# Performance work log

Measured on AMD Instinct MI355X. Metric: run time of the kernel, lower is better.

## Reference

```python
import jax, jax.numpy as jnp
import numpy as np

EPS = 1e-5
STEPS = 4
MULTIPLIER = 4
CROP_SHIFT = 4  # deterministic stand-in for RandomCrop: translate by 4px


def _box_blur(x):
    # 3x3 box blur, reflect padding (kornia RandomBoxBlur default), shape-preserving
    H, W = x.shape[-2], x.shape[-1]
    xp = jnp.pad(x, ((0, 0), (0, 0), (1, 1), (1, 1)), mode='reflect')
    acc = xp[..., 0:H, 0:W]
    for i in range(3):
        for j in range(3):
            if i == 0 and j == 0:
                continue
            acc = acc + xp[..., i:i + H, j:j + W]
    return acc / 9.0


def _mixed_op(h, w):
    # weighted sum over the 7 DA_2D_PRIMITIVES (deterministic versions):
    # none, blur, invert, hflip, vflip, crop(translate), rotate(90 deg)
    return (w[0] * h
            + w[1] * _box_blur(h)
            + w[2] * (1.0 - h)
            + w[3] * jnp.flip(h, axis=-1)
            + w[4] * jnp.flip(h, axis=-2)
            + w[5] * jnp.roll(h, shift=(CROP_SHIFT, CROP_SHIFT), axis=(-2, -1))
            + w[6] * jnp.rot90(h, k=1, axes=(-2, -1)))


def _cell(s0, s1, weights):
    states = [s0, s1]
    offset = 0
    for i in range(STEPS):
        s = states[0] * 0.0
        for j, h in enumerate(states):
            s = s + _mixed_op(h, weights[offset + j])
        offset += len(states)
        states.append(s)
    return jnp.concatenate(states[-MULTIPLIER:], axis=1)


def setup_inputs() -> dict:
    key = jax.random.key(0)
    k1, k2, k3 = jax.random.split(key, 3)
    B, C, H, W = 16, 48, 128, 128
    return {
        'x': jax.random.normal(k1, (B, C, H, W), dtype=jnp.float32),
        'gamma': jnp.ones((C,), dtype=jnp.float32),
        'beta': jnp.zeros((C,), dtype=jnp.float32),
        'alphas_normal': 0.001 * jax.random.normal(k2, (14, 7), dtype=jnp.float32),
        'alphas_reduce': 0.001 * jax.random.normal(k3, (14, 7), dtype=jnp.float32),
    }


def reference(x, gamma, beta, alphas_normal, alphas_reduce):
    # stem: BatchNorm2d in training mode (batch statistics)
    mean = jnp.mean(x, axis=(0, 2, 3), keepdims=True)
    var = jnp.var(x, axis=(0, 2, 3), keepdims=True)
    s = (x - mean) * jax.lax.rsqrt(var + EPS)
    s = s * gamma[None, :, None, None] + beta[None, :, None, None]
    # layers=1: cell 0 is a reduction cell -> uses alphas_reduce
    w = jax.nn.softmax(alphas_reduce, axis=-1)  # [14 edges, 7 ops]
    return _cell(s, s, w)
```

## Files before the change

### kernel.cpp

```cpp
#include <hip/hip_runtime.h>
#include <math.h>

#define NCH 48
#define NB 16
#define PLANE 16384
#define NPLANES 768

#define WS_PSUM  0
#define WS_PSQ   768
#define WS_SCALE 1536
#define WS_SHIFT 1584
#define WS_TAB   1632
#define WS_CONST 1728

typedef _Float16 h2 __attribute__((ext_vector_type(2)));

__global__ __launch_bounds__(256) void stats_kernel(const float* __restrict__ x,
                                                    float* __restrict__ ws) {
  int p = blockIdx.x;
  int t = threadIdx.x;
  const float4* x4 = (const float4*)x + (size_t)p * 4096;
  float s = 0.f, q = 0.f;
  #pragma unroll
  for (int k = 0; k < 16; ++k) {
    float4 v = x4[k * 256 + t];
    s += v.x + v.y + v.z + v.w;
    q += v.x * v.x + v.y * v.y + v.z * v.z + v.w * v.w;
  }
  #pragma unroll
  for (int off = 32; off > 0; off >>= 1) {
    s += __shfl_xor(s, off, 64);
    q += __shfl_xor(q, off, 64);
  }
  __shared__ float red[8];
  int wid = t >> 6, lane = t & 63;
  if (lane == 0) { red[wid] = s; red[4 + wid] = q; }
  __syncthreads();
  if (t == 0) {
    ws[WS_PSUM + p] = red[0] + red[1] + red[2] + red[3];
    ws[WS_PSQ  + p] = red[4] + red[5] + red[6] + red[7];
  }
}

__global__ void prep_kernel(const float* __restrict__ gamma, const float* __restrict__ beta,
                            const float* __restrict__ alphas, float* __restrict__ ws) {
  int t = threadIdx.x;
  if (t < NCH) {
    float s = 0.f, q = 0.f;
    for (int b = 0; b < NB; ++b) {
      s += ws[WS_PSUM + b * NCH + t];
      q += ws[WS_PSQ  + b * NCH + t];
    }
    const float inv = 1.0f / ((float)NB * PLANE);
    float mean = s * inv;
    float var  = q * inv - mean * mean;
    float sc = gamma[t] * rsqrtf(var + 1e-5f);
    ws[WS_SCALE + t] = sc;
    ws[WS_SHIFT + t] = beta[t] - mean * sc;
  }
  if (t == 0) {
    float w[14][7];
    for (int r = 0; r < 14; ++r) {
      float m = -1e30f;
      for (int k = 0; k < 7; ++k) m = fmaxf(m, alphas[r * 7 + k]);
      float sum = 0.f;
      for (int k = 0; k < 7; ++k) { float e = expf(alphas[r * 7 + k] - m); w[r][k] = e; sum += e; }
      float is = 1.0f / sum;
      for (int k = 0; k < 7; ++k) w[r][k] *= is;
    }
    for (int i = 0; i < 96; ++i) ws[WS_TAB + i] = 0.f;
    for (int i = 0; i < 4;  ++i) ws[WS_CONST + i] = 0.f;
    const int map[14][2] = {
      {0,0},{0,0},
      {0,1},{0,1},{1,1},
      {0,2},{0,2},{1,2},{2,2},
      {0,3},{0,3},{1,3},{2,3},{3,3}
    };
    for (int r = 0; r < 14; ++r) {
      int p = map[r][0], tg = map[r][1];
      float* cf = ws + WS_TAB + (p * 4 + tg) * 6;
      cf[0] += w[r][0] - w[r][2];
      cf[1] += w[r][1] * (1.0f / 9.0f);
      cf[2] += w[r][3];
      cf[3] += w[r][4];
      cf[4] += w[r][5];
      cf[5] += w[r][6];
      ws[WS_CONST + tg] += w[r][2];
    }
  }
}


__device__ __forceinline__ float ldshw(const h2* L, int i, int j) {
  int q = (j >> 2) ^ (i & 31);
  h2 p = L[(i << 6) + (q << 1) + ((j & 2) >> 1)];
  return (j & 1) ? (float)p.y : (float)p.x;
}

#define RDQ(L, I, B, M) {                                                      \
  int q_ = (B) ^ ((I) & 31);                                                   \
  h2 p0_ = (L)[((I) << 6) + (q_ << 1)];                                        \
  h2 p1_ = (L)[((I) << 6) + (q_ << 1) + 1];                                    \
  M.x = (float)p0_.x; M.y = (float)p0_.y;                                      \
  M.z = (float)p1_.x; M.w = (float)p1_.y; }

#define WRQ(L, I, B, V) {                                                      \
  int q_ = (B) ^ ((I) & 31);                                                   \
  h2 p0_, p1_;                                                                 \
  p0_.x = (_Float16)V.x; p0_.y = (_Float16)V.y;                                \
  p1_.x = (_Float16)V.z; p1_.y = (_Float16)V.w;                                \
  (L)[((I) << 6) + (q_ << 1)] = p0_;                                           \
  (L)[((I) << 6) + (q_ << 1) + 1] = p1_; }

#define HROW(h, m, lo, hi)                                                     \
  h.x = lo + m.x + m.y; h.y = m.x + m.y + m.z;                                 \
  h.z = m.y + m.z + m.w; h.w = m.z + m.w + hi;

#define FMA4(T, C, M)                                                          \
  T.x += (C) * M.x; T.y += (C) * M.y; T.z += (C) * M.z; T.w += (C) * M.w;

#define BLUR4(T, A, B, Cq)                                                     \
  T.x += c1 * (A.x + B.x + Cq.x); T.y += c1 * (A.y + B.y + Cq.y);              \
  T.z += c1 * (A.z + B.z + Cq.z); T.w += c1 * (A.w + B.w + Cq.w);

#define FLIPL(T, M)                                                            \
  T.x += c2 * M.w; T.y += c2 * M.z; T.z += c2 * M.y; T.w += c2 * M.x;

#define GATHER(L, OI, TYC) {                                                   \
  float4 m, hA, hB, hC; float lo, hi; int ri;                                  \
                                                                      \
  ri = ((OI) == 0) ? 1 : (OI) - 1;                                             \
  RDQ(L, ri, tx, m) lo = ldshw(L, ri, cLo); hi = ldshw(L, ri, cHi);            \
  HROW(hA, m, lo, hi)                                                          \
                                                                      \
  RDQ(L, (OI), tx, m) lo = ldshw(L, (OI), cLo); hi = ldshw(L, (OI), cHi);      \
  FMA4(T0, c0, m)                                                              \
  HROW(hB, m, lo, hi)                                                          \
                                                                      \
  RDQ(L, (OI)+1, tx, m) lo = ldshw(L, (OI)+1, cLo); hi = ldshw(L, (OI)+1, cHi);\
  FMA4(T1, c0, m)                                                              \
  HROW(hC, m, lo, hi)                                                          \
  BLUR4(T0, hA, hB, hC)                                                        \
                                                                      \
  RDQ(L, (OI)+2, tx, m) lo = ldshw(L, (OI)+2, cLo); hi = ldshw(L, (OI)+2, cHi);\
  FMA4(T2, c0, m)                                                              \
  HROW(hA, m, lo, hi)                                                          \
  BLUR4(T1, hB, hC, hA)                                                        \
                                                                      \
  RDQ(L, (OI)+3, tx, m) lo = ldshw(L, (OI)+3, cLo); hi = ldshw(L, (OI)+3, cHi);\
  FMA4(T3, c0, m)                                                              \
  HROW(hB, m, lo, hi)                                                          \
  BLUR4(T2, hC, hA, hB)                                                        \
                                                                      \
  ri = ((OI) == 124) ? 126 : (OI) + 4;                                         \
  RDQ(L, ri, tx, m) lo = ldshw(L, ri, cLo); hi = ldshw(L, ri, cHi);            \
  HROW(hC, m, lo, hi)                                                          \
  BLUR4(T3, hA, hB, hC)                                                        \
                                                                   \
  RDQ(L, (OI),   31 - tx, m) FLIPL(T0, m)                                      \
  RDQ(L, (OI)+1, 31 - tx, m) FLIPL(T1, m)                                      \
  RDQ(L, (OI)+2, 31 - tx, m) FLIPL(T2, m)                                      \
  RDQ(L, (OI)+3, 31 - tx, m) FLIPL(T3, m)                                      \
                                                                   \
  RDQ(L, 127 - (OI), tx, m) FMA4(T0, c3, m)                                    \
  RDQ(L, 126 - (OI), tx, m) FMA4(T1, c3, m)                                    \
  RDQ(L, 125 - (OI), tx, m) FMA4(T2, c3, m)                                    \
  RDQ(L, 124 - (OI), tx, m) FMA4(T3, c3, m)                                    \
                                                              \
  RDQ(L, ((OI) - 4) & 127, rc, m) FMA4(T0, c4, m)                              \
  RDQ(L, ((OI) - 3) & 127, rc, m) FMA4(T1, c4, m)                              \
  RDQ(L, ((OI) - 2) & 127, rc, m) FMA4(T2, c4, m)                              \
  RDQ(L, ((OI) - 1) & 127, rc, m) FMA4(T3, c4, m)                              \
                                     \
  RDQ(L, oj,     31 - (TYC), m)                                                \
  T0.x += c5 * m.w; T1.x += c5 * m.z; T2.x += c5 * m.y; T3.x += c5 * m.x;      \
  RDQ(L, oj + 1, 31 - (TYC), m)                                                \
  T0.y += c5 * m.w; T1.y += c5 * m.z; T2.y += c5 * m.y; T3.y += c5 * m.x;      \
  RDQ(L, oj + 2, 31 - (TYC), m)                                                \
  T0.z += c5 * m.w; T1.z += c5 * m.z; T2.z += c5 * m.y; T3.z += c5 * m.x;      \
  RDQ(L, oj + 3, 31 - (TYC), m)                                                \
  T0.w += c5 * m.w; T1.w += c5 * m.z; T2.w += c5 * m.y; T3.w += c5 * m.x;      \
}

#define LDCF(P, TG) {                                                          \
  const float* cfp = wsf + WS_TAB + ((P) * 4 + (TG)) * 6;                      \
  c0 = cfp[0]; c1 = cfp[1]; c2 = cfp[2]; c3 = cfp[3]; c4 = cfp[4]; c5 = cfp[5]; }

#define SETC(K) {                                                              \
  float cst = wsf[WS_CONST + (K)];                                             \
  T0.x = cst; T0.y = cst; T0.z = cst; T0.w = cst; T1 = T0; T2 = T0; T3 = T0; }

#define STAGE_BN(L, OI) {                                                      \
  float4 v;                                                                    \
  v = x4[((OI)+0)*32 + tx]; v.x = v.x*sc+sh; v.y = v.y*sc+sh; v.z = v.z*sc+sh; \
  v.w = v.w*sc+sh; WRQ(L, (OI)+0, tx, v)                                       \
  v = x4[((OI)+1)*32 + tx]; v.x = v.x*sc+sh; v.y = v.y*sc+sh; v.z = v.z*sc+sh; \
  v.w = v.w*sc+sh; WRQ(L, (OI)+1, tx, v)                                       \
  v = x4[((OI)+2)*32 + tx]; v.x = v.x*sc+sh; v.y = v.y*sc+sh; v.z = v.z*sc+sh; \
  v.w = v.w*sc+sh; WRQ(L, (OI)+2, tx, v)                                       \
  v = x4[((OI)+3)*32 + tx]; v.x = v.x*sc+sh; v.y = v.y*sc+sh; v.z = v.z*sc+sh; \
  v.w = v.w*sc+sh; WRQ(L, (OI)+3, tx, v) }

#define STAGE_OUT(L, TG, OI) {                                                 \
  float4 v;                                                                    \
  v = out4[(pbase + (TG)*NCH)*4096 + ((OI)+0)*32 + tx]; WRQ(L, (OI)+0, tx, v)  \
  v = out4[(pbase + (TG)*NCH)*4096 + ((OI)+1)*32 + tx]; WRQ(L, (OI)+1, tx, v)  \
  v = out4[(pbase + (TG)*NCH)*4096 + ((OI)+2)*32 + tx]; WRQ(L, (OI)+2, tx, v)  \
  v = out4[(pbase + (TG)*NCH)*4096 + ((OI)+3)*32 + tx]; WRQ(L, (OI)+3, tx, v) }

#define WRITEV(TG, OI) {                                                       \
  out4[(pbase + (TG)*NCH)*4096 + ((OI)+0)*32 + tx] = T0;                       \
  out4[(pbase + (TG)*NCH)*4096 + ((OI)+1)*32 + tx] = T1;                       \
  out4[(pbase + (TG)*NCH)*4096 + ((OI)+2)*32 + tx] = T2;                       \
  out4[(pbase + (TG)*NCH)*4096 + ((OI)+3)*32 + tx] = T3; }

#define LOADV(TG, OI) {                                                        \
  T0 = out4[(pbase + (TG)*NCH)*4096 + ((OI)+0)*32 + tx];                       \
  T1 = out4[(pbase + (TG)*NCH)*4096 + ((OI)+1)*32 + tx];                       \
  T2 = out4[(pbase + (TG)*NCH)*4096 + ((OI)+2)*32 + tx];                       \
  T3 = out4[(pbase + (TG)*NCH)*4096 + ((OI)+3)*32 + tx]; }

#define STASHV(L, OI) {                                                        \
  WRQ(L, (OI)+0, tx, T0) WRQ(L, (OI)+1, tx, T1)                                \
  WRQ(L, (OI)+2, tx, T2) WRQ(L, (OI)+3, tx, T3) }

__global__ __launch_bounds__(256, 1)
void main_kernel(const float* __restrict__ x,
                 const float* __restrict__ wsf, float* out)
{
  __shared__ h2 lds[2 * 8192];
  h2* h0 = lds;
  h2* h1 = lds + 8192;
  int bx = blockIdx.x;
  int b = bx / NCH, c = bx % NCH;
  int tid = threadIdx.x;
  int ty = tid >> 5, tx = tid & 31;
  int oj = tx << 2;
  int cLo = (tx == 0)  ? 1   : oj - 1;
  int cHi = (tx == 31) ? 126 : oj + 4;
  int rc  = (tx + 31) & 31;
  float4* out4 = (float4*)out;
  const size_t pbase = (size_t)b * 192 + c;
  const float4* x4 = (const float4*)x + (size_t)bx * 4096;
  float sc = wsf[WS_SCALE + c], sh = wsf[WS_SHIFT + c];

  float4 T0, T1, T2, T3;
  float c0, c1, c2, c3, c4, c5;

  #pragma unroll 1
  for (int k = 0; k < 4; ++k) {
    int oi = (ty + 8 * k) << 2;
    STAGE_BN(h0, oi);
  }
  __syncthreads();

  #pragma unroll 1
  for (int k = 0; k < 4; ++k) {
    int oi = (ty + 8 * k) << 2; int tyc = ty + 8 * k;
    SETC(0); LDCF(0, 0);
    GATHER(h0, oi, tyc);
    WRITEV(0, oi);
    STASHV(h1, oi);
  }
  __syncthreads();

  #pragma unroll 1
  for (int k = 0; k < 4; ++k) {
    int oi = (ty + 8 * k) << 2; int tyc = ty + 8 * k;
    SETC(1); LDCF(0, 1); GATHER(h0, oi, tyc);
             LDCF(1, 1); GATHER(h1, oi, tyc);
    WRITEV(1, oi);
    SETC(2); LDCF(0, 2); GATHER(h0, oi, tyc);
             LDCF(1, 2); GATHER(h1, oi, tyc);
    WRITEV(2, oi);
    SETC(3); LDCF(0, 3); GATHER(h0, oi, tyc);
             LDCF(1, 3); GATHER(h1, oi, tyc);
    WRITEV(3, oi);
  }
  __syncthreads();

  #pragma unroll 1
  for (int k = 0; k < 4; ++k) {
    int oi = (ty + 8 * k) << 2;
    STAGE_OUT(h0, 1, oi);
  }
  __syncthreads();

  #pragma unroll 1
  for (int k = 0; k < 4; ++k) {
    int oi = (ty + 8 * k) << 2; int tyc = ty + 8 * k;
    LOADV(2, oi); LDCF(2, 2); GATHER(h0, oi, tyc); WRITEV(2, oi);
    LOADV(3, oi); LDCF(2, 3); GATHER(h0, oi, tyc); WRITEV(3, oi);
  }
  __syncthreads();

  #pragma unroll 1
  for (int k = 0; k < 4; ++k) {
    int oi = (ty + 8 * k) << 2;
    STAGE_OUT(h1, 2, oi);
  }
  __syncthreads();

  #pragma unroll 1
  for (int k = 0; k < 4; ++k) {
    int oi = (ty + 8 * k) << 2; int tyc = ty + 8 * k;
    LOADV(3, oi); LDCF(3, 3); GATHER(h1, oi, tyc); WRITEV(3, oi);
  }
}

extern "C" void kernel_launch(void* const* d_in, const int* in_sizes, int n_in,
                              void* d_out, int out_size, void* d_ws, size_t ws_size,
                              hipStream_t stream) {
  (void)in_sizes; (void)n_in; (void)out_size; (void)ws_size;
  const float* x     = (const float*)d_in[0];
  const float* gamma = (const float*)d_in[1];
  const float* beta  = (const float*)d_in[2];
  const float* a_red = (const float*)d_in[4];
  float* ws  = (float*)d_ws;
  float* out = (float*)d_out;

  stats_kernel<<<NPLANES, 256, 0, stream>>>(x, ws);
  prep_kernel<<<1, 64, 0, stream>>>(gamma, beta, a_red, ws);
  main_kernel<<<NPLANES, 256, 0, stream>>>(x, ws, out);
}
```

Measured before the change: 120.6 us.

## Keep later-state partial sums in registers instead of reloading from global output

Restructures the main kernel so that each gather of a state plane feeds several output states at once. Partial sums for states 2 and 3 are held in 32 float4 register accumulators across phases rather than written to and reloaded from global memory. This removes repeated LOADV reads, one STAGE_OUT pass and a sync, and fully unrolls the row loops. The cost is much higher register pressure, so the launch bounds are relaxed and waves_per_eu(2) is requested, with a risk of spills.

```diff
diff --git a/kernel.cpp b/kernel.cpp
--- a/kernel.cpp
+++ b/kernel.cpp
@@ -116,17 +116,13 @@
   h.x = lo + m.x + m.y; h.y = m.x + m.y + m.z;                                 \
   h.z = m.y + m.z + m.w; h.w = m.z + m.w + hi;
 
-#define FMA4(T, C, M)                                                          \
-  T.x += (C) * M.x; T.y += (C) * M.y; T.z += (C) * M.z; T.w += (C) * M.w;
-
-#define BLUR4(T, A, B, Cq)                                                     \
-  T.x += c1 * (A.x + B.x + Cq.x); T.y += c1 * (A.y + B.y + Cq.y);              \
-  T.z += c1 * (A.z + B.z + Cq.z); T.w += c1 * (A.w + B.w + Cq.w);
-
-#define FLIPL(T, M)                                                            \
-  T.x += c2 * M.w; T.y += c2 * M.z; T.z += c2 * M.y; T.w += c2 * M.x;
-
-#define GATHER(L, OI, TYC) {                                                   \
+#define FMA4A(ACC, R, OP, M) ACC(R,x,OP,M.x) ACC(R,y,OP,M.y) ACC(R,z,OP,M.z) ACC(R,w,OP,M.w)
+#define FLIPLA(ACC, R, M)    ACC(R,x,2,M.w) ACC(R,y,2,M.z) ACC(R,z,2,M.y) ACC(R,w,2,M.x)
+#define BLUR4A(ACC, R, Ah, Bh, Ch)                                             \
+  ACC(R,x,1,(Ah.x+Bh.x+Ch.x)) ACC(R,y,1,(Ah.y+Bh.y+Ch.y))                      \
+  ACC(R,z,1,(Ah.z+Bh.z+Ch.z)) ACC(R,w,1,(Ah.w+Bh.w+Ch.w))
+
+#define GATHER(L, OI, TYC, ACC) {                                              \
   float4 m, hA, hB, hC; float lo, hi; int ri;                                  \
                                                                       \
   ri = ((OI) == 0) ? 1 : (OI) - 1;                                             \
@@ -134,61 +130,79 @@
   HROW(hA, m, lo, hi)                                                          \
                                                                       \
   RDQ(L, (OI), tx, m) lo = ldshw(L, (OI), cLo); hi = ldshw(L, (OI), cHi);      \
-  FMA4(T0, c0, m)                                                              \
+  FMA4A(ACC, 0, 0, m)                                                          \
   HROW(hB, m, lo, hi)                                                          \
                                                                       \
   RDQ(L, (OI)+1, tx, m) lo = ldshw(L, (OI)+1, cLo); hi = ldshw(L, (OI)+1, cHi);\
-  FMA4(T1, c0, m)                                                              \
+  FMA4A(ACC, 1, 0, m)                                                          \
   HROW(hC, m, lo, hi)                                                          \
-  BLUR4(T0, hA, hB, hC)                                                        \
+  BLUR4A(ACC, 0, hA, hB, hC)                                                   \
                                                                       \
   RDQ(L, (OI)+2, tx, m) lo = ldshw(L, (OI)+2, cLo); hi = ldshw(L, (OI)+2, cHi);\
-  FMA4(T2, c0, m)                                                              \
+  FMA4A(ACC, 2, 0, m)                                                          \
   HROW(hA, m, lo, hi)                                                          \
-  BLUR4(T1, hB, hC, hA)                                                        \
+  BLUR4A(ACC, 1, hB, hC, hA)                                                   \
                                                                       \
   RDQ(L, (OI)+3, tx, m) lo = ldshw(L, (OI)+3, cLo); hi = ldshw(L, (OI)+3, cHi);\
-  FMA4(T3, c0, m)                                                              \
+  FMA4A(ACC, 3, 0, m)                                                          \
   HROW(hB, m, lo, hi)                                                          \
-  BLUR4(T2, hC, hA, hB)                                                        \
+  BLUR4A(ACC, 2, hC, hA, hB)                                                   \
                                                                       \
   ri = ((OI) == 124) ? 126 : (OI) + 4;                                         \
   RDQ(L, ri, tx, m) lo = ldshw(L, ri, cLo); hi = ldshw(L, ri, cHi);            \
   HROW(hC, m, lo, hi)                                                          \
-  BLUR4(T3, hA, hB, hC)                                                        \
+  BLUR4A(ACC, 3, hA, hB, hC)                                                   \
                                                                    \
-  RDQ(L, (OI),   31 - tx, m) FLIPL(T0, m)                                      \
-  RDQ(L, (OI)+1, 31 - tx, m) FLIPL(T1, m)                                      \
-  RDQ(L, (OI)+2, 31 - tx, m) FLIPL(T2, m)                                      \
-  RDQ(L, (OI)+3, 31 - tx, m) FLIPL(T3, m)                                      \
+  RDQ(L, (OI),   31 - tx, m) FLIPLA(ACC, 0, m)                                 \
+  RDQ(L, (OI)+1, 31 - tx, m) FLIPLA(ACC, 1, m)                                 \
+  RDQ(L, (OI)+2, 31 - tx, m) FLIPLA(ACC, 2, m)                                 \
+  RDQ(L, (OI)+3, 31 - tx, m) FLIPLA(ACC, 3, m)                                 \
                                                                    \
-  RDQ(L, 127 - (OI), tx, m) FMA4(T0, c3, m)                                    \
-  RDQ(L, 126 - (OI), tx, m) FMA4(T1, c3, m)                                    \
-  RDQ(L, 125 - (OI), tx, m) FMA4(T2, c3, m)                                    \
-  RDQ(L, 124 - (OI), tx, m) FMA4(T3, c3, m)                                    \
+  RDQ(L, 127 - (OI), tx, m) FMA4A(ACC, 0, 3, m)                                \
+  RDQ(L, 126 - (OI), tx, m) FMA4A(ACC, 1, 3, m)                                \
+  RDQ(L, 125 - (OI), tx, m) FMA4A(ACC, 2, 3, m)                                \
+  RDQ(L, 124 - (OI), tx, m) FMA4A(ACC, 3, 3, m)                                \
                                                               \
-  RDQ(L, ((OI) - 4) & 127, rc, m) FMA4(T0, c4, m)                              \
-  RDQ(L, ((OI) - 3) & 127, rc, m) FMA4(T1, c4, m)                              \
-  RDQ(L, ((OI) - 2) & 127, rc, m) FMA4(T2, c4, m)                              \
-  RDQ(L, ((OI) - 1) & 127, rc, m) FMA4(T3, c4, m)                              \
+  RDQ(L, ((OI) - 4) & 127, rc, m) FMA4A(ACC, 0, 4, m)                          \
+  RDQ(L, ((OI) - 3) & 127, rc, m) FMA4A(ACC, 1, 4, m)                          \
+  RDQ(L, ((OI) - 2) & 127, rc, m) FMA4A(ACC, 2, 4, m)                          \
+  RDQ(L, ((OI) - 1) & 127, rc, m) FMA4A(ACC, 3, 4, m)                          \
                                      \
   RDQ(L, oj,     31 - (TYC), m)                                                \
-  T0.x += c5 * m.w; T1.x += c5 * m.z; T2.x += c5 * m.y; T3.x += c5 * m.x;      \
+  ACC(0,x,5,m.w) ACC(1,x,5,m.z) ACC(2,x,5,m.y) ACC(3,x,5,m.x)                  \
   RDQ(L, oj + 1, 31 - (TYC), m)                                                \
-  T0.y += c5 * m.w; T1.y += c5 * m.z; T2.y += c5 * m.y; T3.y += c5 * m.x;      \
+  ACC(0,y,5,m.w) ACC(1,y,5,m.z) ACC(2,y,5,m.y) ACC(3,y,5,m.x)                  \
   RDQ(L, oj + 2, 31 - (TYC), m)                                                \
-  T0.z += c5 * m.w; T1.z += c5 * m.z; T2.z += c5 * m.y; T3.z += c5 * m.x;      \
+  ACC(0,z,5,m.w) ACC(1,z,5,m.z) ACC(2,z,5,m.y) ACC(3,z,5,m.x)                  \
   RDQ(L, oj + 3, 31 - (TYC), m)                                                \
-  T0.w += c5 * m.w; T1.w += c5 * m.z; T2.w += c5 * m.y; T3.w += c5 * m.x;      \
-}
-
-#define LDCF(P, TG) {                                                          \
-  const float* cfp = wsf + WS_TAB + ((P) * 4 + (TG)) * 6;                      \
-  c0 = cfp[0]; c1 = cfp[1]; c2 = cfp[2]; c3 = cfp[3]; c4 = cfp[4]; c5 = cfp[5]; }
-
-#define SETC(K) {                                                              \
-  float cst = wsf[WS_CONST + (K)];                                             \
-  T0.x = cst; T0.y = cst; T0.z = cst; T0.w = cst; T1 = T0; T2 = T0; T3 = T0; }
+  ACC(0,w,5,m.w) ACC(1,w,5,m.z) ACC(2,w,5,m.y) ACC(3,w,5,m.x)                  \
+}
+
+#define ACC_T(R,Cc,OP,V)  T##R.Cc += wA##OP * (V);
+#define ACC_A0(R,Cc,OP,V) { float v_=(V); T##R.Cc += wA##OP*v_; p40_##R.Cc += wB##OP*v_; p50_##R.Cc += wC##OP*v_; }
+#define ACC_A1(R,Cc,OP,V) { float v_=(V); T##R.Cc += wA##OP*v_; p41_##R.Cc += wB##OP*v_; p51_##R.Cc += wC##OP*v_; }
+#define ACC_A2(R,Cc,OP,V) { float v_=(V); T##R.Cc += wA##OP*v_; p42_##R.Cc += wB##OP*v_; p52_##R.Cc += wC##OP*v_; }
+#define ACC_A3(R,Cc,OP,V) { float v_=(V); T##R.Cc += wA##OP*v_; p43_##R.Cc += wB##OP*v_; p53_##R.Cc += wC##OP*v_; }
+#define ACC_B0(R,Cc,OP,V) { float v_=(V); T##R.Cc += wD##OP*v_; p40_##R.Cc += wB##OP*v_; p50_##R.Cc += wC##OP*v_; }
+#define ACC_B1(R,Cc,OP,V) { float v_=(V); T##R.Cc += wD##OP*v_; p41_##R.Cc += wB##OP*v_; p51_##R.Cc += wC##OP*v_; }
+#define ACC_B2(R,Cc,OP,V) { float v_=(V); T##R.Cc += wD##OP*v_; p42_##R.Cc += wB##OP*v_; p52_##R.Cc += wC##OP*v_; }
+#define ACC_B3(R,Cc,OP,V) { float v_=(V); T##R.Cc += wD##OP*v_; p43_##R.Cc += wB##OP*v_; p53_##R.Cc += wC##OP*v_; }
+#define ACC_C0(R,Cc,OP,V) { float v_=(V); p40_##R.Cc += wA##OP*v_; p50_##R.Cc += wC##OP*v_; }
+#define ACC_C1(R,Cc,OP,V) { float v_=(V); p41_##R.Cc += wA##OP*v_; p51_##R.Cc += wC##OP*v_; }
+#define ACC_C2(R,Cc,OP,V) { float v_=(V); p42_##R.Cc += wA##OP*v_; p52_##R.Cc += wC##OP*v_; }
+#define ACC_C3(R,Cc,OP,V) { float v_=(V); p43_##R.Cc += wA##OP*v_; p53_##R.Cc += wC##OP*v_; }
+#define ACC_D0(R,Cc,OP,V) p50_##R.Cc += wA##OP * (V);
+#define ACC_D1(R,Cc,OP,V) p51_##R.Cc += wA##OP * (V);
+#define ACC_D2(R,Cc,OP,V) p52_##R.Cc += wA##OP * (V);
+#define ACC_D3(R,Cc,OP,V) p53_##R.Cc += wA##OP * (V);
+
+#define LDCFS(PRE, P, TG) {                                                    \
+  const float* cfp_ = wsf + WS_TAB + ((P) * 4 + (TG)) * 6;                     \
+  PRE##0 = cfp_[0]; PRE##1 = cfp_[1]; PRE##2 = cfp_[2];                        \
+  PRE##3 = cfp_[3]; PRE##4 = cfp_[4]; PRE##5 = cfp_[5]; }
+
+#define SETT(VV) { T0 = VV; T1 = VV; T2 = VV; T3 = VV; }
+#define INITP(P, VV) { P##_0 = VV; P##_1 = VV; P##_2 = VV; P##_3 = VV; }
 
 #define STAGE_BN(L, OI) {                                                      \
   float4 v;                                                                    \
@@ -208,23 +222,28 @@
   v = out4[(pbase + (TG)*NCH)*4096 + ((OI)+2)*32 + tx]; WRQ(L, (OI)+2, tx, v)  \
   v = out4[(pbase + (TG)*NCH)*4096 + ((OI)+3)*32 + tx]; WRQ(L, (OI)+3, tx, v) }
 
-#define WRITEV(TG, OI) {                                                       \
+#define WRITET(TG, OI) {                                                       \
   out4[(pbase + (TG)*NCH)*4096 + ((OI)+0)*32 + tx] = T0;                       \
   out4[(pbase + (TG)*NCH)*4096 + ((OI)+1)*32 + tx] = T1;                       \
   out4[(pbase + (TG)*NCH)*4096 + ((OI)+2)*32 + tx] = T2;                       \
   out4[(pbase + (TG)*NCH)*4096 + ((OI)+3)*32 + tx] = T3; }
 
-#define LOADV(TG, OI) {                                                        \
-  T0 = out4[(pbase + (TG)*NCH)*4096 + ((OI)+0)*32 + tx];                       \
-  T1 = out4[(pbase + (TG)*NCH)*4096 + ((OI)+1)*32 + tx];                       \
-  T2 = out4[(pbase + (TG)*NCH)*4096 + ((OI)+2)*32 + tx];                       \
-  T3 = out4[(pbase + (TG)*NCH)*4096 + ((OI)+3)*32 + tx]; }
-
-#define STASHV(L, OI) {                                                        \
+#define WRITEP(P, TG, OI) {                                                    \
+  out4[(pbase + (TG)*NCH)*4096 + ((OI)+0)*32 + tx] = P##_0;                    \
+  out4[(pbase + (TG)*NCH)*4096 + ((OI)+1)*32 + tx] = P##_1;                    \
+  out4[(pbase + (TG)*NCH)*4096 + ((OI)+2)*32 + tx] = P##_2;                    \
+  out4[(pbase + (TG)*NCH)*4096 + ((OI)+3)*32 + tx] = P##_3; }
+
+#define STASHT(L, OI) {                                                        \
   WRQ(L, (OI)+0, tx, T0) WRQ(L, (OI)+1, tx, T1)                                \
   WRQ(L, (OI)+2, tx, T2) WRQ(L, (OI)+3, tx, T3) }
 
-__global__ __launch_bounds__(256, 1)
+#define STASHP(L, P, OI) {                                                     \
+  WRQ(L, (OI)+0, tx, P##_0) WRQ(L, (OI)+1, tx, P##_1)                          \
+  WRQ(L, (OI)+2, tx, P##_2) WRQ(L, (OI)+3, tx, P##_3) }
+
+__global__ __launch_bounds__(256)
+__attribute__((amdgpu_waves_per_eu(2)))
 void main_kernel(const float* __restrict__ x,
                  const float* __restrict__ wsf, float* out)
 {
@@ -244,68 +263,70 @@
   const float4* x4 = (const float4*)x + (size_t)bx * 4096;
   float sc = wsf[WS_SCALE + c], sh = wsf[WS_SHIFT + c];
 
+  const int oiA = ty << 2,  tyA = ty;
+  const int oiB = (ty + 8) << 2,  tyB = ty + 8;
+  const int oiC = (ty + 16) << 2, tyC2 = ty + 16;
+  const int oiD = (ty + 24) << 2, tyD = ty + 24;
+
   float4 T0, T1, T2, T3;
-  float c0, c1, c2, c3, c4, c5;
-
-  #pragma unroll 1
-  for (int k = 0; k < 4; ++k) {
-    int oi = (ty + 8 * k) << 2;
-    STAGE_BN(h0, oi);
-  }
-  __syncthreads();
-
-  #pragma unroll 1
-  for (int k = 0; k < 4; ++k) {
-    int oi = (ty + 8 * k) << 2; int tyc = ty + 8 * k;
-    SETC(0); LDCF(0, 0);
-    GATHER(h0, oi, tyc);
-    WRITEV(0, oi);
-    STASHV(h1, oi);
-  }
-  __syncthreads();
-
-  #pragma unroll 1
-  for (int k = 0; k < 4; ++k) {
-    int oi = (ty + 8 * k) << 2; int tyc = ty + 8 * k;
-    SETC(1); LDCF(0, 1); GATHER(h0, oi, tyc);
-             LDCF(1, 1); GATHER(h1, oi, tyc);
-    WRITEV(1, oi);
-    SETC(2); LDCF(0, 2); GATHER(h0, oi, tyc);
-             LDCF(1, 2); GATHER(h1, oi, tyc);
-    WRITEV(2, oi);
-    SETC(3); LDCF(0, 3); GATHER(h0, oi, tyc);
-             LDCF(1, 3); GATHER(h1, oi, tyc);
-    WRITEV(3, oi);
-  }
-  __syncthreads();
-
-  #pragma unroll 1
-  for (int k = 0; k < 4; ++k) {
-    int oi = (ty + 8 * k) << 2;
-    STAGE_OUT(h0, 1, oi);
-  }
-  __syncthreads();
-
-  #pragma unroll 1
-  for (int k = 0; k < 4; ++k) {
-    int oi = (ty + 8 * k) << 2; int tyc = ty + 8 * k;
-    LOADV(2, oi); LDCF(2, 2); GATHER(h0, oi, tyc); WRITEV(2, oi);
-    LOADV(3, oi); LDCF(2, 3); GATHER(h0, oi, tyc); WRITEV(3, oi);
-  }
-  __syncthreads();
-
-  #pragma unroll 1
-  for (int k = 0; k < 4; ++k) {
-    int oi = (ty + 8 * k) << 2;
-    STAGE_OUT(h1, 2, oi);
-  }
-  __syncthreads();
-
-  #pragma unroll 1
-  for (int k = 0; k < 4; ++k) {
-    int oi = (ty + 8 * k) << 2; int tyc = ty + 8 * k;
-    LOADV(3, oi); LDCF(3, 3); GATHER(h1, oi, tyc); WRITEV(3, oi);
-  }
+  float wA0, wA1, wA2, wA3, wA4, wA5;
+  float wB0, wB1, wB2, wB3, wB4, wB5;
+  float wC0, wC1, wC2, wC3, wC4, wC5;
+  float wD0, wD1, wD2, wD3, wD4, wD5;
+
+  float4 p40_0, p40_1, p40_2, p40_3, p41_0, p41_1, p41_2, p41_3;
+  float4 p42_0, p42_1, p42_2, p42_3, p43_0, p43_1, p43_2, p43_3;
+  float4 p50_0, p50_1, p50_2, p50_3, p51_0, p51_1, p51_2, p51_3;
+  float4 p52_0, p52_1, p52_2, p52_3, p53_0, p53_1, p53_2, p53_3;
+  {
+    float c2_ = wsf[WS_CONST + 2], c3_ = wsf[WS_CONST + 3];
+    float4 v2; v2.x = c2_; v2.y = c2_; v2.z = c2_; v2.w = c2_;
+    float4 v3; v3.x = c3_; v3.y = c3_; v3.z = c3_; v3.w = c3_;
+    INITP(p40, v2) INITP(p41, v2) INITP(p42, v2) INITP(p43, v2)
+    INITP(p50, v3) INITP(p51, v3) INITP(p52, v3) INITP(p53, v3)
+  }
+
+  STAGE_BN(h0, oiA) STAGE_BN(h0, oiB) STAGE_BN(h0, oiC) STAGE_BN(h0, oiD)
+  __syncthreads();
+
+  LDCFS(wA, 0, 0) LDCFS(wB, 0, 2) LDCFS(wC, 0, 3)
+  {
+    float c0_ = wsf[WS_CONST + 0];
+    float4 v0; v0.x = c0_; v0.y = c0_; v0.z = c0_; v0.w = c0_;
+    SETT(v0) GATHER(h0, oiA, tyA, ACC_A0) WRITET(0, oiA) STASHT(h1, oiA)
+    SETT(v0) GATHER(h0, oiB, tyB, ACC_A1) WRITET(0, oiB) STASHT(h1, oiB)
+    SETT(v0) GATHER(h0, oiC, tyC2, ACC_A2) WRITET(0, oiC) STASHT(h1, oiC)
+    SETT(v0) GATHER(h0, oiD, tyD, ACC_A3) WRITET(0, oiD) STASHT(h1, oiD)
+  }
+  __syncthreads();
+
+  LDCFS(wA, 0, 1) LDCFS(wD, 1, 1) LDCFS(wB, 1, 2) LDCFS(wC, 1, 3)
+  {
+    float c1_ = wsf[WS_CONST + 1];
+    float4 v1; v1.x = c1_; v1.y = c1_; v1.z = c1_; v1.w = c1_;
+    SETT(v1) GATHER(h0, oiA, tyA, ACC_T) GATHER(h1, oiA, tyA, ACC_B0) WRITET(1, oiA)
+    SETT(v1) GATHER(h0, oiB, tyB, ACC_T) GATHER(h1, oiB, tyB, ACC_B1) WRITET(1, oiB)
+    SETT(v1) GATHER(h0, oiC, tyC2, ACC_T) GATHER(h1, oiC, tyC2, ACC_B2) WRITET(1, oiC)
+    SETT(v1) GATHER(h0, oiD, tyD, ACC_T) GATHER(h1, oiD, tyD, ACC_B3) WRITET(1, oiD)
+  }
+  __syncthreads();
+
+  STAGE_OUT(h0, 1, oiA) STAGE_OUT(h0, 1, oiB)
+  STAGE_OUT(h0, 1, oiC) STAGE_OUT(h0, 1, oiD)
+  __syncthreads();
+
+  LDCFS(wA, 2, 2) LDCFS(wC, 2, 3)
+  GATHER(h0, oiA, tyA, ACC_C0) WRITEP(p40, 2, oiA) STASHP(h1, p40, oiA)
+  GATHER(h0, oiB, tyB, ACC_C1) WRITEP(p41, 2, oiB) STASHP(h1, p41, oiB)
+  GATHER(h0, oiC, tyC2, ACC_C2) WRITEP(p42, 2, oiC) STASHP(h1, p42, oiC)
+  GATHER(h0, oiD, tyD, ACC_C3) WRITEP(p43, 2, oiD) STASHP(h1, p43, oiD)
+  __syncthreads();
+
+  LDCFS(wA, 3, 3)
+  GATHER(h1, oiA, tyA, ACC_D0) WRITEP(p50, 3, oiA)
+  GATHER(h1, oiB, tyB, ACC_D1) WRITEP(p51, 3, oiB)
+  GATHER(h1, oiC, tyC2, ACC_D2) WRITEP(p52, 3, oiC)
+  GATHER(h1, oiD, tyD, ACC_D3) WRITEP(p53, 3, oiD)
 }
 
 extern "C" void kernel_launch(void* const* d_in, const int* in_sizes, int n_in,
```

New measurement: 251.3 us. 108% more time.
